# Kernel tuning notes

Hardware: AMD Instinct MI355X
Metric: run time of the kernel (lower is better)

The kernel has to match this reference:

```python
import jax, jax.numpy as jnp
import numpy as np

B, N = 128, 256
EPS = float(np.finfo(np.float32).eps)  # torch clamp_probs epsilon for fp32


def to_z(logits, u):
    # torch.distributions.utils.clamp_probs + Gumbel perturbation
    uc = jnp.clip(u, EPS, 1.0 - EPS)
    return logits + (-jnp.log(-jnp.log(uc)))


def _find_cycle(heads):
    # heads[j] = parent of j; node 0 is the root (heads[0] == 0).
    L = len(heads)
    color = np.zeros(L, dtype=np.int8)  # 0 unvisited, 1 on path, 2 done
    color[0] = 2
    for start in range(1, L):
        if color[start]:
            continue
        path = []
        v = start
        while color[v] == 0:
            color[v] = 1
            path.append(v)
            v = int(heads[v])
        if color[v] == 1:  # found a cycle
            i = path.index(v)
            return path[i:]
        for p in path:
            color[p] = 2
    return None


def _chu_liu(score):
    # score[h, d] = weight of edge h -> d; diag and column 0 are -inf.
    L = score.shape[0]
    heads = score.argmax(axis=0)
    heads[0] = 0
    cyc = _find_cycle(heads)
    if cyc is None:
        return heads
    cyc = np.asarray(cyc)
    mask = np.ones(L, dtype=bool)
    mask[cyc] = False
    non = np.where(mask)[0]  # includes root 0
    n = len(non)
    cyc_head_sc = score[heads[cyc], cyc]  # [|C|] chosen in-edge weights of cycle nodes
    # contracted score matrix: nodes = non-cycle nodes + one supernode (index n)
    new = np.full((n + 1, n + 1), -np.inf, dtype=score.dtype)
    new[:n, :n] = score[np.ix_(non, non)]
    into = score[np.ix_(non, cyc)] - cyc_head_sc[None, :]  # gain of entering cycle at each node
    arg_into = into.argmax(axis=1)
    new[:n, n] = into[np.arange(n), arg_into]
    outo = score[np.ix_(cyc, non)]
    arg_out = outo.argmax(axis=0)
    new[n, :n] = outo[arg_out, np.arange(n)]
    nh = _chu_liu(new)
    # expand
    heads_out = np.empty(L, dtype=np.int64)
    nh_non = nh[:n]
    safe = np.clip(nh_non, 0, n - 1)
    heads_out[non] = np.where(nh_non == n, cyc[arg_out], non[safe])
    heads_out[cyc] = heads[cyc]
    hc = int(nh[n])  # head of the contracted supernode (index into non)
    heads_out[cyc[arg_into[hc]]] = non[hc]  # break the cycle at the entry node
    heads_out[0] = 0
    return heads_out


def edmonds_batch(z, lengths):
    # z: np [B, N, N] edge scores z[b, h, d]; root = node 0; per-graph size lengths[b].
    Bn, Nn, _ = z.shape
    arb = np.zeros((Bn, Nn, Nn), dtype=np.float32)
    stats = np.zeros((Bn,), dtype=np.float32)
    for b in range(Bn):  # irregular sequential graph algorithm: per-graph host loop
        L = int(lengths[b])
        s = z[b, :L, :L].astype(np.float64).copy()
        np.fill_diagonal(s, -np.inf)
        s[:, 0] = -np.inf  # no incoming edges to root
        heads = _chu_liu(s)
        deps = np.arange(1, L)
        arb[b, heads[deps], deps] = 1.0
        stats[b] = z[b, heads[deps], deps].sum()
    return jnp.asarray(arb), jnp.asarray(stats)


def setup_inputs():
    key = jax.random.key(0)
    k1, k2, k3 = jax.random.split(key, 3)
    logits = jax.random.normal(k1, (B, N, N), dtype=jnp.float32)
    u = jax.random.uniform(k2, (B, N, N), dtype=jnp.float32)
    lengths = jax.random.randint(k3, (B,), 2, N + 1, dtype=jnp.int32)
    return {"logits": logits, "u": u, "lengths": lengths}


def reference(logits, u, lengths):
    z = to_z(logits, u)  # Gumbel-perturbed scores (differentiable part)
    arb, stats = edmonds_batch(np.asarray(z), np.asarray(lengths))
    return (arb, stats, z)
```

## Files before the change

kernel.cpp:

```cpp
#include <hip/hip_runtime.h>
#include <cmath>

static constexpr int Bn = 128;
static constexpr int Nn = 256;
static constexpr int META_PB = 131072;

template <typename T>
__global__ __launch_bounds__(256) void zinit_kernel(
    const float* __restrict__ logits,
    const float* __restrict__ u,
    float* __restrict__ zout,
    float* __restrict__ arb,
    T* __restrict__ M)
{
    int idx = blockIdx.x * blockDim.x + threadIdx.x;
    int j = idx & (Nn - 1);
    int i = (idx >> 8) & (Nn - 1);
    const float EPS = 1.1920928955078125e-07f;
    float uv = u[idx];
    uv = fminf(fmaxf(uv, EPS), 1.0f - EPS);
    float z = logits[idx] - logf(-logf(uv));
    zout[idx] = z;
    arb[idx] = 0.0f;
    M[idx] = (i == j || j == 0) ? (T)(-INFINITY) : (T)z;
}

template <typename T>
__global__ __launch_bounds__(256) void edmonds_kernel(
    const int* __restrict__ lengths,
    const float* __restrict__ zout,
    T* __restrict__ Mg,
    unsigned char* __restrict__ metag,
    float* __restrict__ arb,
    float* __restrict__ stats)
{
    const int b = blockIdx.x;
    const int t = threadIdx.x;
    const int lane = t & 63, wv = t >> 6;
    T* M = Mg + (size_t)b * (Nn * Nn);
    unsigned char* meta = metag + (size_t)b * META_PB;
    const float* zb = zout + (size_t)b * (Nn * Nn);

    __shared__ unsigned short act[256];
    __shared__ unsigned short h[256];
    __shared__ unsigned short h2[256];
    __shared__ unsigned short p1[256];
    __shared__ unsigned short p2[256];
    __shared__ unsigned short inv_[256];
    __shared__ unsigned short cyc_c[256];
    __shared__ unsigned short non_c[256];
    __shared__ unsigned short cslot_s[256];
    __shared__ unsigned short resc[256];
    __shared__ unsigned short lev_n[256], lev_c[256];
    __shared__ int lev_off[256];
    __shared__ unsigned char in_cyc[256];
    __shared__ T hval[256];
    __shared__ T chs[256];
    __shared__ double red[256];
    __shared__ unsigned wmin[4];
    __shared__ int wcnt[4];
    __shared__ int sh_clen, sh_cnt, sh_wslot;

    const int L = lengths[b];

    act[t] = (unsigned short)t;
    if (t < L) {
        T best = -INFINITY; int bi = 0;
        const T* col = M + t;
        for (int i = 0; i < L; ++i) {
            T v = col[i * Nn];
            if (v > best) { best = v; bi = i; }
        }
        h[t] = (t == 0) ? (unsigned short)0 : (unsigned short)bi;
        hval[t] = best;
    }
    __syncthreads();

    int Lc = L, depth = 0, moff = 0;

    while (true) {
        in_cyc[t] = 0;
        if (t < Lc) p1[t] = h[t];
        __syncthreads();

        const int rounds = 32 - __clz(Lc - 1);
        unsigned short* pa = p1;
        unsigned short* pb = p2;
        for (int r = 0; r < rounds; ++r) {
            if (t < Lc) pb[t] = pa[pa[t]];
            __syncthreads();
            unsigned short* tmp = pa; pa = pb; pb = tmp;
        }

        unsigned cand = (t >= 1 && t < Lc && pa[t] != 0) ? (unsigned)t : 0xFFFFu;
        for (int m = 1; m < 64; m <<= 1)
            cand = min(cand, (unsigned)__shfl_xor((int)cand, m));
        if (lane == 0) wmin[wv] = cand;
        __syncthreads();
        const unsigned vstar = min(min(wmin[0], wmin[1]), min(wmin[2], wmin[3]));
        if (vstar == 0xFFFFu) break;

        if (t == 0) {
            int w = pa[vstar];
            int cl = 0, v = w;
            do { cyc_c[cl++] = (unsigned short)v; in_cyc[v] = 1; v = h[v]; }
            while (v != w);
            sh_clen = cl;
            sh_wslot = act[w];
            sh_cnt = 0;
        }
        __syncthreads();
        const int clen = sh_clen;
        const int n = Lc - clen;
        const int wslot = sh_wslot;

        const bool fl = (t < Lc) && !in_cyc[t];
        unsigned long long mask = __ballot(fl);
        if (lane == 0) wcnt[wv] = __popcll(mask);
        __syncthreads();
        if (fl) {
            int base = 0;
            for (int k = 0; k < wv; ++k) base += wcnt[k];
            int pos = base + __popcll(mask & ((1ull << lane) - 1ull));
            non_c[pos] = (unsigned short)t;
            inv_[t] = (unsigned short)pos;
        }
        if (t < clen) {
            const int cc = cyc_c[t];
            chs[t] = hval[cc];
            cslot_s[t] = act[cc];
        }
        __syncthreads();

        T vin_r = (T)0, vout_r = (T)0;
        unsigned char argin_r = 0, argout_r = 0;
        int slot_r = 0;
        if (t < n) {
            slot_r = act[non_c[t]];
            T bv = -INFINITY; int bi = 0;
            T bo = -INFINITY; int bj = 0;
            for (int c = 0; c < clen; ++c) {
                const int cs = cslot_s[c];
                T vi = M[slot_r * Nn + cs] - chs[c];
                T vo = M[cs * Nn + slot_r];
                if (vi > bv) { bv = vi; bi = c; }
                if (vo > bo) { bo = vo; bj = c; }
            }
            vin_r = bv; argin_r = (unsigned char)bi;
            vout_r = bo; argout_r = (unsigned char)bj;
        }

        unsigned char* mp = meta + moff;
        if (t < n) {
            mp[t] = (unsigned char)non_c[t];
            mp[n + t] = argin_r;
            mp[2 * n + t] = argout_r;
            M[slot_r * Nn + wslot] = vin_r;
            M[wslot * Nn + slot_r] = vout_r;
        }
        if (t < clen) {
            mp[3 * n + t] = (unsigned char)cyc_c[t];
            mp[3 * n + clen + t] = (unsigned char)h[cyc_c[t]];
        }
        if (t == 0) {
            M[wslot * Nn + wslot] = (T)(-INFINITY);
            lev_n[depth] = (unsigned short)n;
            lev_c[depth] = (unsigned short)clen;
            lev_off[depth] = moff;
        }
        unsigned short myact = 0, myh = 0; T myhval = (T)0; bool need = false;
        if (t < n) {
            const int oc = non_c[t];
            myact = act[oc];
            const int ho = h[oc];
            need = (in_cyc[ho] != 0);
            if (!need) { myh = inv_[ho]; myhval = hval[oc]; }
        }
        __syncthreads();

        if (t < n) {
            act[t] = myact;
            if (!need) { h[t] = myh; hval[t] = myhval; }
            else { int kk = atomicAdd(&sh_cnt, 1); resc[kk] = (unsigned short)t; }
        }
        if (t == 0) {
            act[n] = (unsigned short)wslot;
            int kk = atomicAdd(&sh_cnt, 1); resc[kk] = (unsigned short)n;
        }
        __syncthreads();
        moff += 3 * n + 2 * clen;
        ++depth;
        Lc = n + 1;

        const int nr = sh_cnt;
        if (t < nr) {
            const int jc = resc[t];
            const int cslot = act[jc];
            T best = -INFINITY; int bi = 0;
            for (int i = 0; i < Lc; ++i) {
                T v = M[(int)act[i] * Nn + cslot];
                if (v > best) { best = v; bi = i; }
            }
            h[jc] = (unsigned short)bi;
            hval[jc] = best;
        }
        if (t == 0) h[0] = 0;
        __syncthreads();
    }

    unsigned short* hcur = h;
    unsigned short* hnew = h2;
    for (int lvl = depth - 1; lvl >= 0; --lvl) {
        const int n = lev_n[lvl];
        const int c = lev_c[lvl];
        const unsigned char* mp = meta + lev_off[lvl];
        const unsigned char* pnon    = mp;
        const unsigned char* pargin  = mp + n;
        const unsigned char* pargout = mp + 2 * n;
        const unsigned char* pcyc    = mp + 3 * n;
        const unsigned char* phcyc   = mp + 3 * n + c;
        if (t < n) {
            const int x = hcur[t];
            hnew[pnon[t]] = (x == n) ? (unsigned short)pcyc[pargout[t]]
                                     : (unsigned short)pnon[x];
        }
        if (t < c) hnew[pcyc[t]] = phcyc[t];
        __syncthreads();
        if (t == 0) {
            const int hc = hcur[n];
            hnew[pcyc[pargin[hc]]] = pnon[hc];
            hnew[0] = 0;
        }
        __syncthreads();
        unsigned short* tmp = hcur; hcur = hnew; hnew = tmp;
    }

    double acc = 0.0;
    if (t >= 1 && t < L) {
        const int hd = hcur[t];
        arb[(size_t)b * (Nn * Nn) + hd * Nn + t] = 1.0f;
        acc = (double)zb[hd * Nn + t];
    }
    red[t] = acc;
    __syncthreads();
    for (int s = 128; s > 0; s >>= 1) {
        if (t < s) red[t] += red[t + s];
        __syncthreads();
    }
    if (t == 0) stats[b] = (float)red[0];
}

extern "C" void kernel_launch(void* const* d_in, const int* in_sizes, int n_in,
                              void* d_out, int out_size, void* d_ws, size_t ws_size,
                              hipStream_t stream)
{
    const float* logits  = (const float*)d_in[0];
    const float* u       = (const float*)d_in[1];
    const int*   lengths = (const int*)d_in[2];

    float* out   = (float*)d_out;
    float* arb   = out;
    float* stats = out + (size_t)Bn * Nn * Nn;
    float* zout  = stats + Bn;

    const int total = Bn * Nn * Nn;
    const int zblocks = total / 256;

    const size_t needD = (size_t)Bn * Nn * Nn * sizeof(double) + (size_t)Bn * META_PB;

    if (ws_size >= needD) {
        double* M = (double*)d_ws;
        unsigned char* meta = (unsigned char*)d_ws + (size_t)Bn * Nn * Nn * sizeof(double);
        zinit_kernel<double><<<zblocks, 256, 0, stream>>>(logits, u, zout, arb, M);
        edmonds_kernel<double><<<Bn, 256, 0, stream>>>(lengths, zout, M, meta, arb, stats);
    } else {
        float* M = (float*)d_ws;
        unsigned char* meta = (unsigned char*)d_ws + (size_t)Bn * Nn * Nn * sizeof(float);
        zinit_kernel<float><<<zblocks, 256, 0, stream>>>(logits, u, zout, arb, M);
        edmonds_kernel<float><<<Bn, 256, 0, stream>>>(lengths, zout, M, meta, arb, stats);
    }
}
```

Baseline: 774.1 us.

## Move cycle detection pointer-jumping into one wavefront using register shuffles

Cycle detection (pointer doubling over parent arrays, the minimum-candidate reduction and the cycle walk) now runs entirely in wavefront 0. Each lane holds four parent entries in registers and gathers through shuffles, instead of using shared ping-pong buffers with a block barrier every round. This removes about log2(L) block-wide barriers and the extra reduction barrier per contraction iteration. In exchange each doubling round costs 16 shuffles, the other three waves sit idle during detection, and the in_cyc and h[0] resets move to the end of the iteration.

```diff
diff --git a/kernel.cpp b/kernel.cpp
--- a/kernel.cpp
+++ b/kernel.cpp
@@ -25,6 +25,15 @@
     M[idx] = (i == j || j == 0) ? (T)(-INFINITY) : (T)z;
 }
 
+__device__ __forceinline__ int sel4(int v, int a0, int a1, int a2, int a3) {
+    int x0 = __shfl(a0, v & 63);
+    int x1 = __shfl(a1, v & 63);
+    int x2 = __shfl(a2, v & 63);
+    int x3 = __shfl(a3, v & 63);
+    int s = v >> 6;
+    return s == 0 ? x0 : (s == 1 ? x1 : (s == 2 ? x2 : x3));
+}
+
 template <typename T>
 __global__ __launch_bounds__(256) void edmonds_kernel(
     const int* __restrict__ lengths,
@@ -44,8 +53,6 @@
     __shared__ unsigned short act[256];
     __shared__ unsigned short h[256];
     __shared__ unsigned short h2[256];
-    __shared__ unsigned short p1[256];
-    __shared__ unsigned short p2[256];
     __shared__ unsigned short inv_[256];
     __shared__ unsigned short cyc_c[256];
     __shared__ unsigned short non_c[256];
@@ -57,13 +64,13 @@
     __shared__ T hval[256];
     __shared__ T chs[256];
     __shared__ double red[256];
-    __shared__ unsigned wmin[4];
     __shared__ int wcnt[4];
     __shared__ int sh_clen, sh_cnt, sh_wslot;
 
     const int L = lengths[b];
 
     act[t] = (unsigned short)t;
+    in_cyc[t] = 0;
     if (t < L) {
         T best = -INFINITY; int bi = 0;
         const T* col = M + t;
@@ -73,44 +80,53 @@
         }
         h[t] = (t == 0) ? (unsigned short)0 : (unsigned short)bi;
         hval[t] = best;
+    } else {
+        h[t] = 0;
+        hval[t] = (T)0;
     }
     __syncthreads();
 
     int Lc = L, depth = 0, moff = 0;
 
     while (true) {
-        in_cyc[t] = 0;
-        if (t < Lc) p1[t] = h[t];
-        __syncthreads();
-
-        const int rounds = 32 - __clz(Lc - 1);
-        unsigned short* pa = p1;
-        unsigned short* pb = p2;
-        for (int r = 0; r < rounds; ++r) {
-            if (t < Lc) pb[t] = pa[pa[t]];
-            __syncthreads();
-            unsigned short* tmp = pa; pa = pb; pb = tmp;
-        }
-
-        unsigned cand = (t >= 1 && t < Lc && pa[t] != 0) ? (unsigned)t : 0xFFFFu;
-        for (int m = 1; m < 64; m <<= 1)
-            cand = min(cand, (unsigned)__shfl_xor((int)cand, m));
-        if (lane == 0) wmin[wv] = cand;
-        __syncthreads();
-        const unsigned vstar = min(min(wmin[0], wmin[1]), min(wmin[2], wmin[3]));
-        if (vstar == 0xFFFFu) break;
-
-        if (t == 0) {
-            int w = pa[vstar];
-            int cl = 0, v = w;
-            do { cyc_c[cl++] = (unsigned short)v; in_cyc[v] = 1; v = h[v]; }
-            while (v != w);
-            sh_clen = cl;
-            sh_wslot = act[w];
-            sh_cnt = 0;
+        if (wv == 0) {
+            int h0 = h[lane], h1 = h[64 | lane], h2r = h[128 | lane], h3 = h[192 | lane];
+            int p0 = h0, p1 = h1, p2 = h2r, p3 = h3;
+            const int rounds = 32 - __clz(Lc - 1);
+            for (int r = 0; r < rounds; ++r) {
+                int n0 = sel4(p0, p0, p1, p2, p3);
+                int n1 = sel4(p1, p0, p1, p2, p3);
+                int n2 = sel4(p2, p0, p1, p2, p3);
+                int n3 = sel4(p3, p0, p1, p2, p3);
+                p0 = n0; p1 = n1; p2 = n2; p3 = n3;
+            }
+            unsigned cand = 0xFFFFu;
+            if (lane >= 1 && lane < Lc && p0 != 0) cand = (unsigned)lane;
+            { int i1 = 64 | lane;  if (i1 < Lc && p1 != 0) cand = min(cand, (unsigned)i1); }
+            { int i2 = 128 | lane; if (i2 < Lc && p2 != 0) cand = min(cand, (unsigned)i2); }
+            { int i3 = 192 | lane; if (i3 < Lc && p3 != 0) cand = min(cand, (unsigned)i3); }
+            for (int m = 1; m < 64; m <<= 1)
+                cand = min(cand, (unsigned)__shfl((int)cand, (lane ^ m) & 63));
+            if (cand == 0xFFFFu) {
+                if (lane == 0) sh_clen = 0;
+            } else {
+                const int w = sel4((int)cand, p0, p1, p2, p3);
+                int cl = 0, v = w;
+                do {
+                    if (lane == 0) { cyc_c[cl] = (unsigned short)v; in_cyc[v] = 1; }
+                    ++cl;
+                    v = sel4(v, h0, h1, h2r, h3);
+                } while (v != w);
+                if (lane == 0) {
+                    sh_clen = cl;
+                    sh_wslot = act[w];
+                    sh_cnt = 0;
+                }
+            }
         }
         __syncthreads();
         const int clen = sh_clen;
+        if (clen == 0) break;
         const int n = Lc - clen;
         const int wslot = sh_wslot;
 
@@ -118,6 +134,7 @@
         unsigned long long mask = __ballot(fl);
         if (lane == 0) wcnt[wv] = __popcll(mask);
         __syncthreads();
+
         if (fl) {
             int base = 0;
             for (int k = 0; k < wv; ++k) base += wcnt[k];
@@ -149,7 +166,6 @@
             vin_r = bv; argin_r = (unsigned char)bi;
             vout_r = bo; argout_r = (unsigned char)bj;
         }
-
         unsigned char* mp = meta + moff;
         if (t < n) {
             mp[t] = (unsigned char)non_c[t];
@@ -186,7 +202,9 @@
         if (t == 0) {
             act[n] = (unsigned short)wslot;
             int kk = atomicAdd(&sh_cnt, 1); resc[kk] = (unsigned short)n;
-        }
+            h[0] = 0;
+        }
+        in_cyc[t] = 0;
         __syncthreads();
         moff += 3 * n + 2 * clen;
         ++depth;
@@ -204,7 +222,6 @@
             h[jc] = (unsigned short)bi;
             hval[jc] = best;
         }
-        if (t == 0) h[0] = 0;
         __syncthreads();
     }
 
```

Result: slower. 855.1 us (+10.5%).

## Track second-best in-edge to avoid column rescans after cycle contraction

Applied to the files above, without the earlier changes.

Each node now keeps a runner-up parent and its score alongside the best. After a contraction, a node's best head is updated from the surviving best, the runner-up and the new supernode edge, so a full column rescan is needed only when both candidates fell inside the cycle. The supernode's head comes from a wave-shuffle argmax over the computed into-cycle values instead of a serial scan. This adds shared-memory state and branching, and tie-breaking or runner-up staleness could make results differ from a full rescan.

```diff
diff --git a/kernel.cpp b/kernel.cpp
--- a/kernel.cpp
+++ b/kernel.cpp
@@ -55,8 +55,12 @@
     __shared__ int lev_off[256];
     __shared__ unsigned char in_cyc[256];
     __shared__ T hval[256];
+    __shared__ unsigned short r2[256];
+    __shared__ T r2v[256];
     __shared__ T chs[256];
     __shared__ double red[256];
+    __shared__ T sh_sv[4];
+    __shared__ int sh_si[4];
     __shared__ unsigned wmin[4];
     __shared__ int wcnt[4];
     __shared__ int sh_clen, sh_cnt, sh_wslot;
@@ -65,14 +69,19 @@
 
     act[t] = (unsigned short)t;
     if (t < L) {
-        T best = -INFINITY; int bi = 0;
+        T best = -INFINITY; int bi = -1;
+        T sec  = -INFINITY; int si = -1;
         const T* col = M + t;
         for (int i = 0; i < L; ++i) {
             T v = col[i * Nn];
-            if (v > best) { best = v; bi = i; }
-        }
+            if (v > best) { sec = best; si = bi; best = v; bi = i; }
+            else if (v > sec) { sec = v; si = i; }
+        }
+        if (bi < 0) bi = 0;
         h[t] = (t == 0) ? (unsigned short)0 : (unsigned short)bi;
         hval[t] = best;
+        r2[t] = (si < 0) ? (unsigned short)0xFFFF : (unsigned short)si;
+        r2v[t] = sec;
     }
     __syncthreads();
 
@@ -150,6 +159,17 @@
             vout_r = bo; argout_r = (unsigned char)bj;
         }
 
+        {
+            T rv = (t < n) ? vin_r : (T)(-INFINITY);
+            int ri = (t < n) ? t : 0x7FFFFFFF;
+            for (int m = 1; m < 64; m <<= 1) {
+                T ov = __shfl_xor(rv, m);
+                int oi = __shfl_xor(ri, m);
+                if (ov > rv || (ov == rv && oi < ri)) { rv = ov; ri = oi; }
+            }
+            if (lane == 0) { sh_sv[wv] = rv; sh_si[wv] = ri; }
+        }
+
         unsigned char* mp = meta + moff;
         if (t < n) {
             mp[t] = (unsigned char)non_c[t];
@@ -168,24 +188,52 @@
             lev_c[depth] = (unsigned short)clen;
             lev_off[depth] = moff;
         }
-        unsigned short myact = 0, myh = 0; T myhval = (T)0; bool need = false;
+        unsigned short myact = 0;
+        unsigned short nh = 0, nr2 = 0xFFFF;
+        T nhv = (T)0, nr2v = (T)0;
+        bool resFlag = false;
         if (t < n) {
             const int oc = non_c[t];
             myact = act[oc];
             const int ho = h[oc];
-            need = (in_cyc[ho] != 0);
-            if (!need) { myh = inv_[ho]; myhval = hval[oc]; }
+            const T hvalo = hval[oc];
+            const unsigned short r2o = r2[oc];
+            const T r2vo = r2v[oc];
+            const bool hAlive = (in_cyc[ho] == 0);
+            const bool r2Alive = (r2o != 0xFFFF) && (in_cyc[r2o] == 0);
+            const T V = vout_r;
+            if (hAlive) {
+                const unsigned short hoNew = inv_[ho];
+                if (V > hvalo) { nh = (unsigned short)n; nhv = V; nr2 = hoNew; nr2v = hvalo; }
+                else {
+                    nh = hoNew; nhv = hvalo;
+                    if (r2Alive) {
+                        if (V > r2vo) { nr2 = (unsigned short)n; nr2v = V; }
+                        else          { nr2 = inv_[r2o]; nr2v = r2vo; }
+                    } else { nr2 = 0xFFFF; }
+                }
+            } else {
+                if (r2Alive) {
+                    const unsigned short r2New = inv_[r2o];
+                    if (V > r2vo) { nh = (unsigned short)n; nhv = V; nr2 = r2New; nr2v = r2vo; }
+                    else          { nh = r2New; nhv = r2vo; nr2 = 0xFFFF; }
+                } else resFlag = true;
+            }
         }
         __syncthreads();
 
         if (t < n) {
             act[t] = myact;
-            if (!need) { h[t] = myh; hval[t] = myhval; }
+            if (!resFlag) { h[t] = nh; hval[t] = nhv; r2[t] = nr2; r2v[t] = nr2v; }
             else { int kk = atomicAdd(&sh_cnt, 1); resc[kk] = (unsigned short)t; }
         }
         if (t == 0) {
             act[n] = (unsigned short)wslot;
-            int kk = atomicAdd(&sh_cnt, 1); resc[kk] = (unsigned short)n;
+            T bv = sh_sv[0]; int bi = sh_si[0];
+            for (int w2 = 1; w2 < 4; ++w2)
+                if (sh_sv[w2] > bv) { bv = sh_sv[w2]; bi = sh_si[w2]; }
+            h[n] = (unsigned short)bi; hval[n] = bv; r2[n] = 0xFFFF;
+            h[0] = 0;
         }
         __syncthreads();
         moff += 3 * n + 2 * clen;
@@ -196,15 +244,19 @@
         if (t < nr) {
             const int jc = resc[t];
             const int cslot = act[jc];
-            T best = -INFINITY; int bi = 0;
+            T best = -INFINITY; int bi = -1;
+            T sec  = -INFINITY; int si = -1;
             for (int i = 0; i < Lc; ++i) {
                 T v = M[(int)act[i] * Nn + cslot];
-                if (v > best) { best = v; bi = i; }
+                if (v > best) { sec = best; si = bi; best = v; bi = i; }
+                else if (v > sec) { sec = v; si = i; }
             }
+            if (bi < 0) bi = 0;
             h[jc] = (unsigned short)bi;
             hval[jc] = best;
-        }
-        if (t == 0) h[0] = 0;
+            r2[jc] = (si < 0) ? (unsigned short)0xFFFF : (unsigned short)si;
+            r2v[jc] = sec;
+        }
         __syncthreads();
     }
 
```

After: 1.451 ms. 87.4% more time.
